# Kernel optimization log

Measured on AMD Instinct MI355X. Metric: run time of the kernel, lower is better.

## Reference

```python
import jax, jax.numpy as jnp
import numpy as np

DIM = 192
NUM_HEADS = 8
EPS = 1e-12  # torch F.normalize default eps


def setup_inputs() -> dict:
    key = jax.random.key(0)
    k1, k2, k3, k4 = jax.random.split(key, 4)
    b, c, h, w = 8, DIM, 128, 128
    x = jax.random.normal(k1, (b, c, h, w), dtype=jnp.float32)
    # 1x1 qkv conv weight, stored as (3c, c)
    w_qkv = jax.random.normal(k2, (3 * c, c), dtype=jnp.float32) * (1.0 / np.sqrt(c))
    # depthwise 3x3 conv weight, groups = 3c -> OIHW (3c, 1, 3, 3)
    w_dw = jax.random.normal(k3, (3 * c, 1, 3, 3), dtype=jnp.float32) * (1.0 / 3.0)
    # 1x1 project_out weight (c, c)
    w_out = jax.random.normal(k4, (c, c), dtype=jnp.float32) * (1.0 / np.sqrt(c))
    temperature = jnp.ones((NUM_HEADS, 1, 1), dtype=jnp.float32)
    return {"x": x, "w_qkv": w_qkv, "w_dw": w_dw, "w_out": w_out,
            "temperature": temperature}


def _mdta(x, w_qkv, w_dw, w_out, temperature):
    b, c, h, w = x.shape
    nh = NUM_HEADS
    # 1x1 conv == channel GEMM
    qkv = jnp.einsum('oc,bchw->bohw', w_qkv, x)
    # depthwise 3x3 conv, groups = 3c
    qkv = jax.lax.conv_general_dilated(
        qkv, w_dw, window_strides=(1, 1), padding='SAME',
        feature_group_count=3 * c,
        dimension_numbers=('NCHW', 'OIHW', 'NCHW'))
    q, k, v = jnp.split(qkv, 3, axis=1)
    hd = c // nh
    q = q.reshape(b, nh, hd, h * w)
    k = k.reshape(b, nh, hd, h * w)
    v = v.reshape(b, nh, hd, h * w)
    # L2 normalize over spatial (hw) dim
    q = q / jnp.maximum(jnp.linalg.norm(q, axis=-1, keepdims=True), EPS)
    k = k / jnp.maximum(jnp.linalg.norm(k, axis=-1, keepdims=True), EPS)
    # channel x channel attention per head: (b, nh, hd, hd)
    attn = jnp.einsum('bhcn,bhdn->bhcd', q, k) * temperature
    attn = jax.nn.softmax(attn, axis=-1)
    out = jnp.einsum('bhcd,bhdn->bhcn', attn, v).reshape(b, c, h, w)
    return jnp.einsum('oc,bchw->bohw', w_out, out)


def reference(x, w_qkv, w_dw, w_out, temperature):
    return _mdta(x, w_qkv, w_dw, w_out, temperature)
```

## Files before the change

kernel.cpp:

```cpp
#include <hip/hip_runtime.h>


#define HW 16384
#define WIMG 128
#define C 192
#define C3 576
#define NH 8
#define HD 24

typedef unsigned short ushort8_t __attribute__((ext_vector_type(8)));
typedef unsigned short ushort4_t __attribute__((ext_vector_type(4)));
typedef short short8_t __attribute__((ext_vector_type(8)));
typedef float float4_t __attribute__((ext_vector_type(4)));

__device__ __forceinline__ float bfu2f(unsigned short u) {
    union { unsigned int i; float f; } v; v.i = ((unsigned int)u) << 16; return v.f;
}
__device__ __forceinline__ unsigned short f2bfu(float f) {
    union { float f; unsigned int i; } v; v.f = f;
    unsigned int x = v.i;
    return (unsigned short)((x + 0x7FFFu + ((x >> 16) & 1u)) >> 16);
}
__device__ __forceinline__ float inload(const void* p, int idx, int isbf) {
    return isbf ? bfu2f(((const unsigned short*)p)[idx]) : ((const float*)p)[idx];
}

__device__ __forceinline__ int afrag_idx(int o, int dg) {
    return ((((o >> 4) * 6 + (dg >> 5)) * 4 + ((dg >> 3) & 3)) << 7)
           + ((o & 15) << 3) + (dg & 7);
}

__global__ void probe_dtype(const unsigned int* __restrict__ x, int* __restrict__ flag) {
    const int t = threadIdx.x;
    int cnt = 0;
    for (int i = t; i < 512; i += 256) {
        const unsigned int u = x[i] & 0xFFFFu;
        const unsigned int e = (u >> 7) & 0xFFu;
        if (u == 0u || (e >= 100u && e <= 140u)) cnt++;
    }
#pragma unroll
    for (int off = 32; off; off >>= 1) cnt += __shfl_down(cnt, off, 64);
    __shared__ int s[4];
    if ((t & 63) == 0) s[t >> 6] = cnt;
    __syncthreads();
    if (t == 0) flag[0] = (s[0] + s[1] + s[2] + s[3] > 300) ? 1 : 0;
}

__global__ void prep(const void* __restrict__ wqkv, const void* __restrict__ wdw,
                     const void* __restrict__ wout, const void* __restrict__ temp,
                     const int* __restrict__ flagp, unsigned short* __restrict__ wqb,
                     float* __restrict__ wdwf, float* __restrict__ woutf,
                     float* __restrict__ tempf, float* __restrict__ Sraw,
                     float* __restrict__ normsum) {
    const int isbf = flagp[0];
    const int id = blockIdx.x * 256 + threadIdx.x;
    const int stride = gridDim.x * 256;
    for (int i = id; i < C3 * C; i += stride) {
        const int o = i / C, dg = i - o * C;
        const unsigned short v =
            isbf ? ((const unsigned short*)wqkv)[i] : f2bfu(((const float*)wqkv)[i]);
        wqb[afrag_idx(o, dg)] = v;
    }
    for (int i = id; i < C3 * 9; i += stride) wdwf[i] = inload(wdw, i, isbf);
    for (int i = id; i < C * C; i += stride) woutf[i] = inload(wout, i, isbf);
    for (int i = id; i < NH; i += stride) tempf[i] = inload(temp, i, isbf);
    for (int i = id; i < 8 * NH * HD * HD; i += stride) Sraw[i] = 0.f;
    for (int i = id; i < 8 * 2 * C; i += stride) normsum[i] = 0.f;
}

__global__ __launch_bounds__(512) void gemm_mfma(
    const void* __restrict__ Bsrc, const unsigned short* __restrict__ Abf,
    void* __restrict__ outp, const int* __restrict__ flagp,
    size_t b_batch_stride, size_t b_const_off, size_t o_batch_stride,
    int a_batch_stride, int m_tiles, int b_mode, int out_mode) {
    __shared__ unsigned short sbuf[16384];
    const int isbf = flagp[0];
    const int b_isbf = b_mode | isbf;
    const int tid = threadIdx.x;
    const int batch = blockIdx.y;
    const int n0 = blockIdx.x * 128;
    const size_t b_off = b_batch_stride * batch + b_const_off;
    const size_t o_off = o_batch_stride * batch;
    const unsigned short* Ab = Abf + (size_t)a_batch_stride * batch;

    const int w = tid >> 6;
    const int lane = tid & 63;
    const int l15 = lane & 15;
    const int quad = lane >> 4;
    const int mhalf = w & 1;
    const int nquad = w >> 1;

    short8_t bfr[6][2];
#pragma unroll
    for (int h = 0; h < 2; h++) {
        if (h) __syncthreads();
        if (tid < 192) {
            const int cg = tid >> 4;
            const int pg = tid & 15;
            const int chbase = h * 96 + cg * 8;
            ushort8_t rows[8];
            if (b_isbf) {
                const unsigned short* bp = (const unsigned short*)Bsrc + b_off + n0 + pg * 8;
#pragma unroll
                for (int r = 0; r < 8; r++)
                    rows[r] = *reinterpret_cast<const ushort8_t*>(bp + (size_t)(chbase + r) * HW);
            } else {
                const float* bp = (const float*)Bsrc + b_off + n0 + pg * 8;
#pragma unroll
                for (int r = 0; r < 8; r++) {
                    const float4_t f0 = *reinterpret_cast<const float4_t*>(bp + (size_t)(chbase + r) * HW);
                    const float4_t f1 = *reinterpret_cast<const float4_t*>(bp + (size_t)(chbase + r) * HW + 4);
#pragma unroll
                    for (int i = 0; i < 4; i++) { rows[r][i] = f2bfu(f0[i]); rows[r][i + 4] = f2bfu(f1[i]); }
                }
            }
#pragma unroll
            for (int s = 0; s < 8; s++) {
                ushort8_t outv;
#pragma unroll
                for (int r = 0; r < 8; r++) outv[r] = rows[r][s];
                const int p = pg * 8 + s;
                const int cidx = p * 16 + (cg ^ s);
                *reinterpret_cast<ushort8_t*>(&sbuf[cidx * 8]) = outv;
            }
        }
        __syncthreads();
#pragma unroll
        for (int ksl = 0; ksl < 3; ksl++) {
            const int ks = h * 3 + ksl;
            const int cgl = ks * 4 + quad - h * 12;
#pragma unroll
            for (int nt = 0; nt < 2; nt++) {
                const int p = nquad * 32 + nt * 16 + l15;
                const int cidx = p * 16 + (cgl ^ (p & 7));
                bfr[ks][nt] = *reinterpret_cast<const short8_t*>(&sbuf[cidx * 8]);
            }
        }
    }

    const int o_isbf = out_mode ? isbf : 1;
    const int rr = tid >> 3;
    const int kk = tid & 7;
    for (int mt0 = 0; mt0 < m_tiles; mt0++) {
        const int m0 = mt0 * 64;
        short8_t afr[2][6];
#pragma unroll
        for (int mt = 0; mt < 2; mt++) {
            const int tile = mt0 * 4 + mhalf * 2 + mt;
#pragma unroll
            for (int ks = 0; ks < 6; ks++)
                afr[mt][ks] = *reinterpret_cast<const short8_t*>(
                    Ab + (size_t)((((tile * 6 + ks) << 2) + quad) << 7) + (l15 << 3));
        }
        float4_t acc[2][2];
#pragma unroll
        for (int mt = 0; mt < 2; mt++)
#pragma unroll
            for (int nt = 0; nt < 2; nt++) {
                float4_t z = {0.f, 0.f, 0.f, 0.f};
                acc[mt][nt] = z;
            }
#pragma unroll
        for (int ks = 0; ks < 6; ks++)
#pragma unroll
            for (int mt = 0; mt < 2; mt++)
#pragma unroll
                for (int nt = 0; nt < 2; nt++)
                    acc[mt][nt] = __builtin_amdgcn_mfma_f32_16x16x32_bf16(
                        afr[mt][ks], bfr[ks][nt], acc[mt][nt], 0, 0, 0);
        if (out_mode == 0) {
#pragma unroll
            for (int mt = 0; mt < 2; mt++) {
                const int ch4 = (m0 >> 2) + (mhalf * 2 + mt) * 4 + quad;
#pragma unroll
                for (int nt = 0; nt < 2; nt++) {
                    const int px = n0 + nquad * 32 + nt * 16 + l15;
                    ushort4_t v;
#pragma unroll
                    for (int r = 0; r < 4; r++) v[r] = f2bfu(acc[mt][nt][r]);
                    *reinterpret_cast<ushort4_t*>(
                        (unsigned short*)outp + o_off + ((size_t)ch4 * HW + px) * 4) = v;
                }
            }
        } else if (o_isbf) {
            __syncthreads();
#pragma unroll
            for (int mt = 0; mt < 2; mt++) {
                const int row64 = (mhalf * 2 + mt) * 16 + quad * 4;
#pragma unroll
                for (int nt = 0; nt < 2; nt++) {
                    const int col = nquad * 32 + nt * 16 + l15;
#pragma unroll
                    for (int r = 0; r < 4; r++)
                        sbuf[(row64 + r) * 136 + col] = f2bfu(acc[mt][nt][r]);
                }
            }
            __syncthreads();
            const ushort8_t v0 = *reinterpret_cast<const ushort8_t*>(&sbuf[rr * 136 + kk * 16]);
            const ushort8_t v1 = *reinterpret_cast<const ushort8_t*>(&sbuf[rr * 136 + kk * 16 + 8]);
            unsigned short* op = (unsigned short*)outp + o_off + (size_t)(m0 + rr) * HW + n0 + kk * 16;
            *reinterpret_cast<ushort8_t*>(op) = v0;
            *reinterpret_cast<ushort8_t*>(op + 8) = v1;
        } else {
#pragma unroll
            for (int mt = 0; mt < 2; mt++) {
                const int row = m0 + (mhalf * 2 + mt) * 16 + quad * 4;
#pragma unroll
                for (int nt = 0; nt < 2; nt++) {
                    const int col = n0 + nquad * 32 + nt * 16 + l15;
#pragma unroll
                    for (int r = 0; r < 4; r++)
                        ((float*)outp)[o_off + (size_t)(row + r) * HW + col] = acc[mt][nt][r];
                }
            }
        }
    }
}

__global__ __launch_bounds__(256) void dwconv(
    const unsigned short* __restrict__ qkv0i, const float* __restrict__ wdwf,
    unsigned short* __restrict__ qkv1, float* __restrict__ normsum) {
    const int cg4 = blockIdx.y;
    const int b = blockIdx.z;
    const size_t ibase = ((size_t)b * 144 + cg4) * HW * 4;
    __shared__ float wsm[36];
    if (threadIdx.x < 36) wsm[threadIdx.x] = wdwf[cg4 * 36 + threadIdx.x];
    __syncthreads();
    const int p = blockIdx.x * 2048 + threadIdx.x * 8;
    const int y = p >> 7, x0 = p & 127;
    float acc[4][8];
#pragma unroll
    for (int r = 0; r < 4; r++)
#pragma unroll
        for (int j = 0; j < 8; j++) acc[r][j] = 0.f;
#pragma unroll
    for (int dy = 0; dy < 3; dy++) {
        const int yy = y + dy - 1;
        if (yy < 0 || yy > 127) continue;
        const int rb = yy * WIMG + x0;
        float f[4][10];
#pragma unroll
        for (int m = 0; m < 4; m++) {
            const ushort8_t mm =
                *reinterpret_cast<const ushort8_t*>(qkv0i + ibase + (size_t)(rb + 2 * m) * 4);
#pragma unroll
            for (int r = 0; r < 4; r++) {
                f[r][1 + 2 * m] = bfu2f(mm[r]);
                f[r][2 + 2 * m] = bfu2f(mm[4 + r]);
            }
        }
        if (x0 > 0) {
            const ushort4_t el =
                *reinterpret_cast<const ushort4_t*>(qkv0i + ibase + (size_t)(rb - 1) * 4);
#pragma unroll
            for (int r = 0; r < 4; r++) f[r][0] = bfu2f(el[r]);
        } else {
#pragma unroll
            for (int r = 0; r < 4; r++) f[r][0] = 0.f;
        }
        if (x0 < 120) {
            const ushort4_t er =
                *reinterpret_cast<const ushort4_t*>(qkv0i + ibase + (size_t)(rb + 8) * 4);
#pragma unroll
            for (int r = 0; r < 4; r++) f[r][9] = bfu2f(er[r]);
        } else {
#pragma unroll
            for (int r = 0; r < 4; r++) f[r][9] = 0.f;
        }
#pragma unroll
        for (int r = 0; r < 4; r++) {
            const float w0 = wsm[r * 9 + dy * 3], w1 = wsm[r * 9 + dy * 3 + 1],
                        w2 = wsm[r * 9 + dy * 3 + 2];
#pragma unroll
            for (int j = 0; j < 8; j++)
                acc[r][j] += w0 * f[r][j] + w1 * f[r][j + 1] + w2 * f[r][j + 2];
        }
    }
#pragma unroll
    for (int r = 0; r < 4; r++) {
        ushort8_t outv;
#pragma unroll
        for (int j = 0; j < 8; j++) outv[j] = f2bfu(acc[r][j]);
        *reinterpret_cast<ushort8_t*>(
            qkv1 + ((size_t)b * C3 + cg4 * 4 + r) * HW + p) = outv;
    }
    if (cg4 < 96) {
        float ss[4];
#pragma unroll
        for (int r = 0; r < 4; r++) {
            float s = 0.f;
#pragma unroll
            for (int j = 0; j < 8; j++) s += acc[r][j] * acc[r][j];
            ss[r] = s;
        }
#pragma unroll
        for (int off = 32; off; off >>= 1)
#pragma unroll
            for (int r = 0; r < 4; r++) ss[r] += __shfl_down(ss[r], off, 64);
        if ((threadIdx.x & 63) == 0)
#pragma unroll
            for (int r = 0; r < 4; r++)
                atomicAdd(&normsum[b * 2 * C + cg4 * 4 + r], ss[r]);
    }
}

__global__ __launch_bounds__(256) void attn_gram(
    const unsigned short* __restrict__ qkv1, float* __restrict__ Sraw) {
    const int b = blockIdx.z, h = blockIdx.y;
    const int wave = threadIdx.x >> 6;
    const int lane = threadIdx.x & 63;
    const int l15 = lane & 15, quad = lane >> 4;
    const int k0 = (blockIdx.x * 4 + wave) * 512;
    const unsigned short* qrow = qkv1 + (size_t)b * C3 * HW + (size_t)(h * HD) * HW;
    const unsigned short* krow = qkv1 + (size_t)b * C3 * HW + (size_t)(C + h * HD) * HW;

    float4_t acc[2][2];
#pragma unroll
    for (int mt = 0; mt < 2; mt++)
#pragma unroll
        for (int nt = 0; nt < 2; nt++) {
            float4_t z = {0.f, 0.f, 0.f, 0.f};
            acc[mt][nt] = z;
        }

#pragma unroll 4
    for (int ks = 0; ks < 16; ks++) {
        const int kk = k0 + ks * 32 + quad * 8;
        short8_t qa[2], kb[2];
        qa[0] = *reinterpret_cast<const short8_t*>(qrow + (size_t)l15 * HW + kk);
        qa[1] = *reinterpret_cast<const short8_t*>(qrow + (size_t)(16 + l15) * HW + kk);
        kb[0] = *reinterpret_cast<const short8_t*>(krow + (size_t)l15 * HW + kk);
        kb[1] = *reinterpret_cast<const short8_t*>(krow + (size_t)(16 + l15) * HW + kk);
#pragma unroll
        for (int mt = 0; mt < 2; mt++)
#pragma unroll
            for (int nt = 0; nt < 2; nt++)
                acc[mt][nt] = __builtin_amdgcn_mfma_f32_16x16x32_bf16(
                    qa[mt], kb[nt], acc[mt][nt], 0, 0, 0);
    }

    float* Sb = Sraw + (size_t)b * NH * HD * HD + (size_t)h * HD * HD;
#pragma unroll
    for (int nt = 0; nt < 2; nt++) {
        const int j = nt * 16 + l15;
        if (j >= HD) continue;
#pragma unroll
        for (int mt = 0; mt < 2; mt++) {
            const int i0 = mt * 16 + quad * 4;
#pragma unroll
            for (int r = 0; r < 4; r++) {
                const int i = i0 + r;
                if (i < HD) atomicAdd(&Sb[i * HD + j], acc[mt][nt][r]);
            }
        }
    }
}

__global__ void buildM(const float* __restrict__ Sraw, const float* __restrict__ normsum,
                       const float* __restrict__ tempf, const float* __restrict__ woutf,
                       unsigned short* __restrict__ Mb) {
    __shared__ float As[NH * HD * HD];
    __shared__ float inv[2 * C];
    const int b = blockIdx.y;
    const int tid = threadIdx.x;
    for (int r = tid; r < 2 * C; r += 256)
        inv[r] = 1.f / fmaxf(sqrtf(normsum[b * 2 * C + r]), 1e-12f);
    __syncthreads();
    for (int e = tid; e < NH * HD * HD; e += 256) {
        const int h = e / (HD * HD);
        const int rm = e - h * HD * HD;
        const int i = rm / HD, j = rm % HD;
        As[e] = Sraw[(size_t)b * NH * HD * HD + e] * inv[h * HD + i] * inv[C + h * HD + j] * tempf[h];
    }
    __syncthreads();
    if (tid < C) {
        const int h = tid / HD, i = tid % HD;
        float* rp = As + h * HD * HD + i * HD;
        float mx = -1e30f;
#pragma unroll
        for (int j = 0; j < HD; j++) mx = fmaxf(mx, rp[j]);
        float sum = 0.f;
#pragma unroll
        for (int j = 0; j < HD; j++) { rp[j] = __expf(rp[j] - mx); sum += rp[j]; }
        const float is = 1.f / sum;
#pragma unroll
        for (int j = 0; j < HD; j++) rp[j] *= is;
    }
    __syncthreads();
    const int idx = blockIdx.x * 256 + tid;
    const int o = idx / C, dg = idx % C;
    const int h = dg / HD, d = dg % HD;
    const float* wp = woutf + o * C + h * HD;
    const float* Ap = As + h * HD * HD + d;
    float acc = 0.f;
#pragma unroll
    for (int c2 = 0; c2 < HD; c2++) acc += wp[c2] * Ap[c2 * HD];
    Mb[(size_t)b * C * C + afrag_idx(o, dg)] = f2bfu(acc);
}

extern "C" void kernel_launch(void* const* d_in, const int* in_sizes, int n_in,
                              void* d_out, int out_size, void* d_ws, size_t ws_size,
                              hipStream_t stream) {
    const void* x    = d_in[0];
    const void* wqkv = d_in[1];
    const void* wdw  = d_in[2];
    const void* wout = d_in[3];
    const void* temp = d_in[4];

    char* w = (char*)d_ws;
    int* flag = (int*)w;                          w += 64;
    unsigned short* wqb = (unsigned short*)w;     w += (size_t)C3 * C * 2;
    unsigned short* Mb  = (unsigned short*)w;     w += (size_t)8 * C * C * 2;
    float* wdwf  = (float*)w;                     w += (size_t)C3 * 9 * 4;
    float* woutf = (float*)w;                     w += (size_t)C * C * 4;
    float* tempf = (float*)w;                     w += 64;
    float* normsum = (float*)w;                   w += (size_t)8 * 2 * C * 4;
    float* Sraw  = (float*)w;                     w += (size_t)8 * NH * HD * HD * 4;
    unsigned short* qkv0 = (unsigned short*)w;    w += (size_t)8 * C3 * HW * 2;
    unsigned short* qkv1 = (unsigned short*)w;

    probe_dtype<<<1, 256, 0, stream>>>((const unsigned int*)x, flag);
    prep<<<432, 256, 0, stream>>>(wqkv, wdw, wout, temp, flag, wqb, wdwf, woutf,
                                  tempf, Sraw, normsum);
    gemm_mfma<<<dim3(HW / 128, 8), 512, 0, stream>>>(
        x, wqb, qkv0, flag, (size_t)C * HW, 0, (size_t)C3 * HW, 0, 9, 0, 0);
    dwconv<<<dim3(8, 144, 8), 256, 0, stream>>>(qkv0, wdwf, qkv1, normsum);
    attn_gram<<<dim3(8, NH, 8), 256, 0, stream>>>(qkv1, Sraw);
    buildM<<<dim3(144, 8), 256, 0, stream>>>(Sraw, normsum, tempf, woutf, Mb);
    gemm_mfma<<<dim3(HW / 128, 8), 512, 0, stream>>>(
        qkv1, Mb, d_out, flag, (size_t)C3 * HW, (size_t)2 * C * HW, (size_t)C * HW,
        C * C, 3, 1, 1);
}
```

Baseline: 392.0 us.

## Restructure dwconv to row-per-wave with shuffles and make gram use LDS partials

```diff
diff --git a/kernel.cpp b/kernel.cpp
--- a/kernel.cpp
+++ b/kernel.cpp
@@ -50,8 +50,7 @@
                      const void* __restrict__ wout, const void* __restrict__ temp,
                      const int* __restrict__ flagp, unsigned short* __restrict__ wqb,
                      float* __restrict__ wdwf, float* __restrict__ woutf,
-                     float* __restrict__ tempf, float* __restrict__ Sraw,
-                     float* __restrict__ normsum) {
+                     float* __restrict__ tempf, float* __restrict__ normsum) {
     const int isbf = flagp[0];
     const int id = blockIdx.x * 256 + threadIdx.x;
     const int stride = gridDim.x * 256;
@@ -64,7 +63,6 @@
     for (int i = id; i < C3 * 9; i += stride) wdwf[i] = inload(wdw, i, isbf);
     for (int i = id; i < C * C; i += stride) woutf[i] = inload(wout, i, isbf);
     for (int i = id; i < NH; i += stride) tempf[i] = inload(temp, i, isbf);
-    for (int i = id; i < 8 * NH * HD * HD; i += stride) Sraw[i] = 0.f;
     for (int i = id; i < 8 * 2 * C; i += stride) normsum[i] = 0.f;
 }
 
@@ -222,97 +220,85 @@
     unsigned short* __restrict__ qkv1, float* __restrict__ normsum) {
     const int cg4 = blockIdx.y;
     const int b = blockIdx.z;
+    const int t = threadIdx.x;
+    const int wave = t >> 6, lane = t & 63;
+    const int y = blockIdx.x * 4 + wave;
+    const int px0 = lane * 2;
     const size_t ibase = ((size_t)b * 144 + cg4) * HW * 4;
-    __shared__ float wsm[36];
-    if (threadIdx.x < 36) wsm[threadIdx.x] = wdwf[cg4 * 36 + threadIdx.x];
-    __syncthreads();
-    const int p = blockIdx.x * 2048 + threadIdx.x * 8;
-    const int y = p >> 7, x0 = p & 127;
-    float acc[4][8];
-#pragma unroll
-    for (int r = 0; r < 4; r++)
-#pragma unroll
-        for (int j = 0; j < 8; j++) acc[r][j] = 0.f;
+    const float* wp = wdwf + cg4 * 36;
+
+    float acc[4][2];
+#pragma unroll
+    for (int c = 0; c < 4; c++) { acc[c][0] = 0.f; acc[c][1] = 0.f; }
+
 #pragma unroll
     for (int dy = 0; dy < 3; dy++) {
         const int yy = y + dy - 1;
         if (yy < 0 || yy > 127) continue;
-        const int rb = yy * WIMG + x0;
-        float f[4][10];
-#pragma unroll
-        for (int m = 0; m < 4; m++) {
-            const ushort8_t mm =
-                *reinterpret_cast<const ushort8_t*>(qkv0i + ibase + (size_t)(rb + 2 * m) * 4);
-#pragma unroll
-            for (int r = 0; r < 4; r++) {
-                f[r][1 + 2 * m] = bfu2f(mm[r]);
-                f[r][2 + 2 * m] = bfu2f(mm[4 + r]);
-            }
-        }
-        if (x0 > 0) {
-            const ushort4_t el =
-                *reinterpret_cast<const ushort4_t*>(qkv0i + ibase + (size_t)(rb - 1) * 4);
-#pragma unroll
-            for (int r = 0; r < 4; r++) f[r][0] = bfu2f(el[r]);
-        } else {
-#pragma unroll
-            for (int r = 0; r < 4; r++) f[r][0] = 0.f;
-        }
-        if (x0 < 120) {
-            const ushort4_t er =
-                *reinterpret_cast<const ushort4_t*>(qkv0i + ibase + (size_t)(rb + 8) * 4);
-#pragma unroll
-            for (int r = 0; r < 4; r++) f[r][9] = bfu2f(er[r]);
-        } else {
-#pragma unroll
-            for (int r = 0; r < 4; r++) f[r][9] = 0.f;
-        }
-#pragma unroll
-        for (int r = 0; r < 4; r++) {
-            const float w0 = wsm[r * 9 + dy * 3], w1 = wsm[r * 9 + dy * 3 + 1],
-                        w2 = wsm[r * 9 + dy * 3 + 2];
-#pragma unroll
-            for (int j = 0; j < 8; j++)
-                acc[r][j] += w0 * f[r][j] + w1 * f[r][j + 1] + w2 * f[r][j + 2];
-        }
-    }
-#pragma unroll
-    for (int r = 0; r < 4; r++) {
-        ushort8_t outv;
-#pragma unroll
-        for (int j = 0; j < 8; j++) outv[j] = f2bfu(acc[r][j]);
-        *reinterpret_cast<ushort8_t*>(
-            qkv1 + ((size_t)b * C3 + cg4 * 4 + r) * HW + p) = outv;
+        const ushort8_t m = *reinterpret_cast<const ushort8_t*>(
+            qkv0i + ibase + (size_t)(yy * WIMG + px0) * 4);
+        float fm0[4], fm1[4];
+#pragma unroll
+        for (int c = 0; c < 4; c++) { fm0[c] = bfu2f(m[c]); fm1[c] = bfu2f(m[4 + c]); }
+#pragma unroll
+        for (int c = 0; c < 4; c++) {
+            float lf = __shfl_up(fm1[c], 1, 64);
+            float rf = __shfl_down(fm0[c], 1, 64);
+            if (lane == 0) lf = 0.f;
+            if (lane == 63) rf = 0.f;
+            const float w0 = wp[c * 9 + dy * 3], w1 = wp[c * 9 + dy * 3 + 1],
+                        w2 = wp[c * 9 + dy * 3 + 2];
+            acc[c][0] += w0 * lf + w1 * fm0[c] + w2 * fm1[c];
+            acc[c][1] += w0 * fm0[c] + w1 * fm1[c] + w2 * rf;
+        }
+    }
+#pragma unroll
+    for (int c = 0; c < 4; c++) {
+        const unsigned int pk =
+            (unsigned int)f2bfu(acc[c][0]) | ((unsigned int)f2bfu(acc[c][1]) << 16);
+        *reinterpret_cast<unsigned int*>(
+            qkv1 + ((size_t)b * C3 + cg4 * 4 + c) * HW + y * WIMG + px0) = pk;
     }
     if (cg4 < 96) {
         float ss[4];
 #pragma unroll
-        for (int r = 0; r < 4; r++) {
-            float s = 0.f;
-#pragma unroll
-            for (int j = 0; j < 8; j++) s += acc[r][j] * acc[r][j];
-            ss[r] = s;
-        }
+        for (int c = 0; c < 4; c++) ss[c] = acc[c][0] * acc[c][0] + acc[c][1] * acc[c][1];
 #pragma unroll
         for (int off = 32; off; off >>= 1)
 #pragma unroll
-            for (int r = 0; r < 4; r++) ss[r] += __shfl_down(ss[r], off, 64);
-        if ((threadIdx.x & 63) == 0)
-#pragma unroll
-            for (int r = 0; r < 4; r++)
-                atomicAdd(&normsum[b * 2 * C + cg4 * 4 + r], ss[r]);
-    }
-}
-
+            for (int c = 0; c < 4; c++) ss[c] += __shfl_down(ss[c], off, 64);
+        __shared__ float red[4][4];
+        if (lane == 0)
+#pragma unroll
+            for (int c = 0; c < 4; c++) red[wave][c] = ss[c];
+        __syncthreads();
+        if (t < 4)
+            atomicAdd(&normsum[b * 2 * C + cg4 * 4 + t],
+                      red[0][t] + red[1][t] + red[2][t] + red[3][t]);
+    }
+}
+
+#define AG_LROW 264
 __global__ __launch_bounds__(256) void attn_gram(
-    const unsigned short* __restrict__ qkv1, float* __restrict__ Sraw) {
+    const unsigned short* __restrict__ qkv1, float* __restrict__ Spart) {
+    __shared__ unsigned short qk[2 * 32 * AG_LROW];
     const int b = blockIdx.z, h = blockIdx.y;
-    const int wave = threadIdx.x >> 6;
-    const int lane = threadIdx.x & 63;
+    const int t = threadIdx.x;
+    const size_t qbase0 = (size_t)b * C3 * HW + (size_t)(h * HD) * HW;
+    const size_t kbase0 = qbase0 + (size_t)C * HW;
+    const int wave = t >> 6, lane = t & 63;
     const int l15 = lane & 15, quad = lane >> 4;
-    const int k0 = (blockIdx.x * 4 + wave) * 512;
-    const unsigned short* qrow = qkv1 + (size_t)b * C3 * HW + (size_t)(h * HD) * HW;
-    const unsigned short* krow = qkv1 + (size_t)b * C3 * HW + (size_t)(C + h * HD) * HW;
+
+    for (int s = t; s < 2 * 8 * 33; s += 256) {
+        const int tt = s / (8 * 33);
+        const int rm = s - tt * (8 * 33);
+        const int row = 24 + rm / 33;
+        const int c16 = rm % 33;
+        ushort8_t z;
+#pragma unroll
+        for (int i = 0; i < 8; i++) z[i] = 0;
+        *reinterpret_cast<ushort8_t*>(&qk[(tt * 32 + row) * AG_LROW + c16 * 8]) = z;
+    }
 
     float4_t acc[2][2];
 #pragma unroll
@@ -323,40 +309,72 @@
             acc[mt][nt] = z;
         }
 
-#pragma unroll 4
-    for (int ks = 0; ks < 16; ks++) {
-        const int kk = k0 + ks * 32 + quad * 8;
-        short8_t qa[2], kb[2];
-        qa[0] = *reinterpret_cast<const short8_t*>(qrow + (size_t)l15 * HW + kk);
-        qa[1] = *reinterpret_cast<const short8_t*>(qrow + (size_t)(16 + l15) * HW + kk);
-        kb[0] = *reinterpret_cast<const short8_t*>(krow + (size_t)l15 * HW + kk);
-        kb[1] = *reinterpret_cast<const short8_t*>(krow + (size_t)(16 + l15) * HW + kk);
+    for (int cc = 0; cc < 4; cc++) {
+        const int k0 = (blockIdx.x * 4 + cc) * 256;
+        __syncthreads();
+#pragma unroll
+        for (int it = 0; it < 6; it++) {
+            const int s = it * 256 + t;
+            const int tt = s >= 768;
+            const int rm = s - tt * 768;
+            const int row = rm >> 5;
+            const int c16 = rm & 31;
+            const ushort8_t v = *reinterpret_cast<const ushort8_t*>(
+                qkv1 + (tt ? kbase0 : qbase0) + k0 + (size_t)row * HW + c16 * 8);
+            *reinterpret_cast<ushort8_t*>(&qk[(tt * 32 + row) * AG_LROW + c16 * 8]) = v;
+        }
+        __syncthreads();
+#pragma unroll
+        for (int ks = 0; ks < 2; ks++) {
+            const int kkk = wave * 64 + ks * 32 + quad * 8;
+            short8_t qa[2], kb[2];
+#pragma unroll
+            for (int mt = 0; mt < 2; mt++)
+                qa[mt] = *reinterpret_cast<const short8_t*>(
+                    &qk[(mt * 16 + l15) * AG_LROW + kkk]);
+#pragma unroll
+            for (int nt = 0; nt < 2; nt++)
+                kb[nt] = *reinterpret_cast<const short8_t*>(
+                    &qk[(32 + nt * 16 + l15) * AG_LROW + kkk]);
+#pragma unroll
+            for (int mt = 0; mt < 2; mt++)
+#pragma unroll
+                for (int nt = 0; nt < 2; nt++)
+                    acc[mt][nt] = __builtin_amdgcn_mfma_f32_16x16x32_bf16(
+                        qa[mt], kb[nt], acc[mt][nt], 0, 0, 0);
+        }
+    }
+
+    __syncthreads();
+    float* fs = (float*)qk;
+#pragma unroll
+    for (int mt = 0; mt < 2; mt++)
+#pragma unroll
+        for (int nt = 0; nt < 2; nt++)
+#pragma unroll
+            for (int r = 0; r < 4; r++)
+                fs[((mt * 2 + nt) * 4 + r) * 256 + t] = acc[mt][nt][r];
+    __syncthreads();
+    if (t < 64) {
+        float* Sb = Spart + (((size_t)blockIdx.x * 8 + b) * 8 + h) * (HD * HD);
 #pragma unroll
         for (int mt = 0; mt < 2; mt++)
 #pragma unroll
-            for (int nt = 0; nt < 2; nt++)
-                acc[mt][nt] = __builtin_amdgcn_mfma_f32_16x16x32_bf16(
-                    qa[mt], kb[nt], acc[mt][nt], 0, 0, 0);
-    }
-
-    float* Sb = Sraw + (size_t)b * NH * HD * HD + (size_t)h * HD * HD;
-#pragma unroll
-    for (int nt = 0; nt < 2; nt++) {
-        const int j = nt * 16 + l15;
-        if (j >= HD) continue;
-#pragma unroll
-        for (int mt = 0; mt < 2; mt++) {
-            const int i0 = mt * 16 + quad * 4;
-#pragma unroll
-            for (int r = 0; r < 4; r++) {
-                const int i = i0 + r;
-                if (i < HD) atomicAdd(&Sb[i * HD + j], acc[mt][nt][r]);
-            }
-        }
-    }
-}
-
-__global__ void buildM(const float* __restrict__ Sraw, const float* __restrict__ normsum,
+            for (int nt = 0; nt < 2; nt++) {
+                const int j = nt * 16 + l15;
+#pragma unroll
+                for (int r = 0; r < 4; r++) {
+                    const int i = mt * 16 + quad * 4 + r;
+                    const int q2 = (mt * 2 + nt) * 4 + r;
+                    const float v = fs[q2 * 256 + t] + fs[q2 * 256 + 64 + t] +
+                                    fs[q2 * 256 + 128 + t] + fs[q2 * 256 + 192 + t];
+                    if (i < HD && j < HD) Sb[i * HD + j] = v;
+                }
+            }
+    }
+}
+
+__global__ void buildM(const float* __restrict__ Spart, const float* __restrict__ normsum,
                        const float* __restrict__ tempf, const float* __restrict__ woutf,
                        unsigned short* __restrict__ Mb) {
     __shared__ float As[NH * HD * HD];
@@ -370,7 +388,11 @@
         const int h = e / (HD * HD);
         const int rm = e - h * HD * HD;
         const int i = rm / HD, j = rm % HD;
-        As[e] = Sraw[(size_t)b * NH * HD * HD + e] * inv[h * HD + i] * inv[C + h * HD + j] * tempf[h];
+        float s = 0.f;
+#pragma unroll
+        for (int sp = 0; sp < 16; sp++)
+            s += Spart[(((size_t)sp * 8 + b) * 8 + h) * (HD * HD) + rm];
+        As[e] = s * inv[h * HD + i] * inv[C + h * HD + j] * tempf[h];
     }
     __syncthreads();
     if (tid < C) {
@@ -415,18 +437,18 @@
     float* woutf = (float*)w;                     w += (size_t)C * C * 4;
     float* tempf = (float*)w;                     w += 64;
     float* normsum = (float*)w;                   w += (size_t)8 * 2 * C * 4;
-    float* Sraw  = (float*)w;                     w += (size_t)8 * NH * HD * HD * 4;
+    float* Spart = (float*)w;                     w += (size_t)16 * 8 * NH * HD * HD * 4;
     unsigned short* qkv0 = (unsigned short*)w;    w += (size_t)8 * C3 * HW * 2;
     unsigned short* qkv1 = (unsigned short*)w;
 
     probe_dtype<<<1, 256, 0, stream>>>((const unsigned int*)x, flag);
     prep<<<432, 256, 0, stream>>>(wqkv, wdw, wout, temp, flag, wqb, wdwf, woutf,
-                                  tempf, Sraw, normsum);
+                                  tempf, normsum);
     gemm_mfma<<<dim3(HW / 128, 8), 512, 0, stream>>>(
         x, wqb, qkv0, flag, (size_t)C * HW, 0, (size_t)C3 * HW, 0, 9, 0, 0);
-    dwconv<<<dim3(8, 144, 8), 256, 0, stream>>>(qkv0, wdwf, qkv1, normsum);
-    attn_gram<<<dim3(8, NH, 8), 256, 0, stream>>>(qkv1, Sraw);
-    buildM<<<dim3(144, 8), 256, 0, stream>>>(Sraw, normsum, tempf, woutf, Mb);
+    dwconv<<<dim3(32, 144, 8), 256, 0, stream>>>(qkv0, wdwf, qkv1, normsum);
+    attn_gram<<<dim3(16, NH, 8), 256, 0, stream>>>(qkv1, Spart);
+    buildM<<<dim3(144, 8), 256, 0, stream>>>(Spart, normsum, tempf, woutf, Mb);
     gemm_mfma<<<dim3(HW / 128, 8), 512, 0, stream>>>(
         qkv1, Mb, d_out, flag, (size_t)C3 * HW, (size_t)2 * C * HW, (size_t)C * HW,
         C * C, 3, 1, 1);
```

Measured after the change: 394.0 us. Within noise of the previous version (+0.5%).
